# Kernel tuning notes

Measured on AMD Instinct MI355X. Metric: run time of the kernel, lower is better.

Reference implementation:

```python
import jax, jax.numpy as jnp
import numpy as np

NUM_EMOTIONS = 8
EMOTION_DIM = 32
MAX_EMOTIONS = 3
HIDDEN = 768
NUM_HEADS = 8
HEAD_DIM = HIDDEN // NUM_HEADS // 2  # 48
DEPTH = 0
LAMBDA_INIT = 0.8 - 0.6 * float(np.exp(-0.3 * DEPTH))  # 0.2
EPS = 1e-5


def setup_inputs() -> dict:
    key = jax.random.key(0)
    ks = jax.random.split(key, 16)
    B = 16384
    emotion_indices = jax.random.randint(ks[0], (B, MAX_EMOTIONS), 0, NUM_EMOTIONS)
    confidence_values = jax.random.uniform(ks[1], (B, MAX_EMOTIONS), dtype=jnp.float32)
    emb_table = jax.random.normal(ks[2], (NUM_EMOTIONS + 1, EMOTION_DIM), jnp.float32)
    emb_table = emb_table.at[NUM_EMOTIONS].set(0.0)  # padding_idx row
    s1 = 1.0 / np.sqrt(EMOTION_DIM)
    s2 = 1.0 / np.sqrt(HIDDEN)
    W1 = jax.random.normal(ks[3], (EMOTION_DIM, HIDDEN), jnp.float32) * s1
    b1 = jnp.zeros((HIDDEN,), jnp.float32)
    ln_g = jnp.ones((HIDDEN,), jnp.float32)
    ln_b = jnp.zeros((HIDDEN,), jnp.float32)
    Wq = jax.random.normal(ks[4], (HIDDEN, HIDDEN), jnp.float32) * s2
    Wk = jax.random.normal(ks[5], (HIDDEN, HIDDEN), jnp.float32) * s2
    Wv = jax.random.normal(ks[6], (HIDDEN, HIDDEN), jnp.float32) * s2
    Wo = jax.random.normal(ks[7], (HIDDEN, HIDDEN), jnp.float32) * s2
    lq1 = jax.random.normal(ks[8], (HEAD_DIM,), jnp.float32) * 0.1
    lk1 = jax.random.normal(ks[9], (HEAD_DIM,), jnp.float32) * 0.1
    lq2 = jax.random.normal(ks[10], (HEAD_DIM,), jnp.float32) * 0.1
    lk2 = jax.random.normal(ks[11], (HEAD_DIM,), jnp.float32) * 0.1
    subln_w = jnp.ones((2 * HEAD_DIM,), jnp.float32)
    return dict(emotion_indices=emotion_indices, confidence_values=confidence_values,
                emb_table=emb_table, W1=W1, b1=b1, ln_g=ln_g, ln_b=ln_b,
                Wq=Wq, Wk=Wk, Wv=Wv, Wo=Wo,
                lq1=lq1, lk1=lk1, lq2=lq2, lk2=lk2, subln_w=subln_w)


def _rotary_tables(seq_len, dim):
    inv_freq = 1.0 / (10000.0 ** (jnp.arange(0, dim, 2, dtype=jnp.float32) / dim))  # [dim/2]
    t = jnp.arange(seq_len, dtype=jnp.float32)
    ang = jnp.outer(t, inv_freq)  # [S, dim/2]
    return jnp.cos(ang), jnp.sin(ang)


def _apply_rope(x, cos, sin):
    # x: [B, S, H, D]; cos/sin: [S, D/2] (interleaved pairs)
    x1, x2 = x[..., 0::2], x[..., 1::2]
    c = cos[None, :, None, :]
    s = sin[None, :, None, :]
    r1 = x1 * c - x2 * s
    r2 = x1 * s + x2 * c
    return jnp.stack([r1, r2], axis=-1).reshape(x.shape)


def _forward(emotion_indices, confidence_values, emb_table, W1, b1, ln_g, ln_b,
             Wq, Wk, Wv, Wo, lq1, lk1, lq2, lk2, subln_w):
    B, S = emotion_indices.shape  # S == MAX_EMOTIONS
    idx = jnp.where(emotion_indices < 0, NUM_EMOTIONS, emotion_indices)

    # embedding lookup + confidence weighting
    emb = emb_table[idx] * confidence_values[..., None]  # [B,S,32]

    # Linear + LayerNorm + GELU (dropout = identity in eval)
    h = emb @ W1 + b1  # [B,S,768]
    mu = jnp.mean(h, axis=-1, keepdims=True)
    var = jnp.mean(jnp.square(h - mu), axis=-1, keepdims=True)
    h = (h - mu) / jnp.sqrt(var + EPS) * ln_g + ln_b
    h = jax.nn.gelu(h, approximate=False)

    # rotary tables
    cos, sin = _rotary_tables(S, HEAD_DIM)

    # additive attention mask: -inf over padded key columns
    pad = (idx == NUM_EMOTIONS)  # [B,S]
    neg_inf = jnp.asarray(-jnp.inf, h.dtype)
    mask = jnp.where(pad[:, None, None, :], neg_inf, 0.0)  # [B,1,1,S] -> bcast to [B,1,S,S]

    # differential attention
    q = (h @ Wq).reshape(B, S, 2 * NUM_HEADS, HEAD_DIM)
    k = (h @ Wk).reshape(B, S, 2 * NUM_HEADS, HEAD_DIM)
    v = (h @ Wv).reshape(B, S, NUM_HEADS, 2 * HEAD_DIM)
    q = _apply_rope(q, cos, sin)
    k = _apply_rope(k, cos, sin)

    scale = HEAD_DIM ** -0.5
    scores = jnp.einsum('bqhd,bkhd->bhqk', q, k) * scale + mask  # [B,2H,S,S]
    attn = jax.nn.softmax(scores, axis=-1)
    attn = attn.reshape(B, NUM_HEADS, 2, S, S)
    lam = (jnp.exp(jnp.sum(lq1 * lk1)) - jnp.exp(jnp.sum(lq2 * lk2)) + LAMBDA_INIT)
    diff = attn[:, :, 0] - lam * attn[:, :, 1]  # [B,H,S,S]

    out = jnp.einsum('bhqk,bkhd->bqhd', diff, v)  # [B,S,H,2d]
    # sublayer RMSNorm over last dim
    rms = jnp.sqrt(jnp.mean(jnp.square(out), axis=-1, keepdims=True) + EPS)
    out = out / rms * subln_w
    out = out * (1.0 - LAMBDA_INIT)
    out = out.reshape(B, S, HIDDEN) @ Wo  # [B,S,768]

    # masked mean pooling over non-padding positions
    npad = (~pad).astype(out.dtype)[..., None]  # [B,S,1]
    summed = jnp.sum(out * npad, axis=1)
    denom = jnp.maximum(jnp.sum(npad, axis=1), 1.0)
    return summed / denom  # [B,768]


def reference(emotion_indices, confidence_values, emb_table, W1, b1, ln_g, ln_b,
              Wq, Wk, Wv, Wo, lq1, lk1, lq2, lk2, subln_w):
    return _forward(emotion_indices, confidence_values, emb_table, W1, b1, ln_g, ln_b,
                    Wq, Wk, Wv, Wo, lq1, lk1, lq2, lk2, subln_w)
```

## Files before the change

### kernel.cpp

```cpp
#include <hip/hip_runtime.h>
#include <hip/hip_bf16.h>
#include <math.h>
#include <stdint.h>

typedef __hip_bfloat16 bf16;
typedef __attribute__((ext_vector_type(8))) short short8;
typedef __attribute__((ext_vector_type(4))) float f32x4;
typedef __attribute__((ext_vector_type(2))) unsigned int u32x2;

#define NB 16384
#define HID 768
#define EPS_LN 1e-5f
#define LAM_INIT 0.2f

__device__ __forceinline__ float bf2f(bf16 x){ return __bfloat162float(x); }
__device__ __forceinline__ bf16  f2bf(float x){ return __float2bfloat16(x); }
__device__ __forceinline__ float bfbits(uint32_t lo16){ return __uint_as_float(lo16 << 16); }
__device__ __forceinline__ uint32_t f2bfbits(float x){
  union { float f; uint32_t u; } v; v.f = x;
  uint32_t u = v.u;
  uint32_t r = (u + 0x7fff + ((u >> 16) & 1)) >> 16;
  return r;
}

template<typename T> __device__ __forceinline__ float ldv(const void* p, int i);
template<> __device__ __forceinline__ float ldv<float>(const void* p, int i){ return ((const float*)p)[i]; }
template<> __device__ __forceinline__ float ldv<bf16 >(const void* p, int i){ return bf2f(((const bf16*)p)[i]); }

template<typename T> __device__ __forceinline__ void stv(T* p, float v);
template<> __device__ __forceinline__ void stv<float>(float* p, float v){ *p = v; }
template<> __device__ __forceinline__ void stv<bf16 >(bf16*  p, float v){ *p = f2bf(v); }

__device__ __forceinline__ void async_copy16(void* lds, const void* g){
  __builtin_amdgcn_global_load_lds(
      (const __attribute__((address_space(1))) unsigned int*)g,
      (__attribute__((address_space(3))) unsigned int*)lds, 16, 0, 0);
}

__device__ __forceinline__ float wred64(float v){
  #pragma unroll
  for (int m = 1; m <= 32; m <<= 1) v += __shfl_xor(v, m, 64);
  return v;
}

__device__ __forceinline__ int detect_bf(const void* etab){
  const uint32_t* p = (const uint32_t*)((const char*)etab + 512);
  uint32_t v = 0;
  #pragma unroll
  for (int i = 0; i < 16; ++i) v |= p[i];
  return v == 0u ? 1 : 0;
}


__device__ __forceinline__ void misc_body(int isbf, const void* lq1, const void* lk1,
                                          const void* lq2, const void* lk2, float* prep){
  const int lane = threadIdx.x;
  if (lane >= 64) return;
  if (lane == 0) ((int*)prep)[0] = isbf;

  float p1 = 0.f, p2 = 0.f;
  if (lane < 48){
    if (isbf){ p1 = ldv<bf16>(lq1,lane)*ldv<bf16>(lk1,lane); p2 = ldv<bf16>(lq2,lane)*ldv<bf16>(lk2,lane); }
    else     { p1 = ldv<float>(lq1,lane)*ldv<float>(lk1,lane); p2 = ldv<float>(lq2,lane)*ldv<float>(lk2,lane); }
  }
  p1 = wred64(p1); p2 = wred64(p2);
  if (lane == 0) prep[1] = expf(p1) - expf(p2) + LAM_INIT;

  if (lane < 24){
    float invf = powf(10000.f, -(float)(2*lane)/48.f);
    #pragma unroll
    for (int s=0;s<3;++s){
      float ang = (float)s*invf;
      float c = cosf(ang), sv = sinf(ang);
      prep[16  + s*32 + lane] = c;
      prep[128 + s*32 + lane] = sv;
      prep[256 + (s*24 + lane)*2    ] = c;
      prep[256 + (s*24 + lane)*2 + 1] = sv;
    }
  }
}

template<typename T>
__device__ __forceinline__ void prep_e1_body(int id, const void* etab, const void* W1,
                                             const void* b1, float* prep,
                                             float (*red)[4]){
  const int tid = threadIdx.x;
  const int wave = tid >> 6, lane = tid & 63;

  float et[32];
  #pragma unroll
  for (int e=0;e<32;++e) et[e] = ldv<T>(etab, id*32+e);

  float su=0.f, suu=0.f, sub=0.f;
  #pragma unroll
  for (int q=0;q<3;++q){
    const int cc = tid + q*256;
    float s = 0.f;
    #pragma unroll
    for (int e=0;e<32;++e) s += et[e]*ldv<T>(W1, e*HID+cc);
    prep[1024 + id*HID + cc] = s;
    float bv = ldv<T>(b1, cc);
    su += s; suu += s*s; sub += s*bv;
  }
  su = wred64(su); suu = wred64(suu); sub = wred64(sub);
  if (lane==0){ red[0][wave]=su; red[1][wave]=suu; red[2][wave]=sub; }
  __syncthreads();
  if (tid==0){
    float a=0.f,b=0.f,c=0.f;
    #pragma unroll
    for (int w=0;w<4;++w){ a+=red[0][w]; b+=red[1][w]; c+=red[2][w]; }
    prep[512+id]=a*(1.f/768.f); prep[528+id]=b*(1.f/768.f); prep[544+id]=c*(1.f/768.f);
  }
  if (id==0){
    float sb=0.f, sbb=0.f;
    #pragma unroll
    for (int q=0;q<3;++q){ float bv=ldv<T>(b1, tid+q*256); sb+=bv; sbb+=bv*bv; }
    sb=wred64(sb); sbb=wred64(sbb);
    __syncthreads();
    if (lane==0){ red[0][wave]=sb; red[1][wave]=sbb; }
    __syncthreads();
    if (tid==0){
      float a=0.f,b=0.f;
      #pragma unroll
      for (int w=0;w<4;++w){ a+=red[0][w]; b+=red[1][w]; }
      prep[560]=a*(1.f/768.f); prep[561]=b*(1.f/768.f);
    }
  }
}

template<typename T>
__device__ __forceinline__ void transpose_body(bf16 (*tile)[33], const void* src,
                                               bf16* dst, int n0, int k0){
  const int tid = threadIdx.x;
  const int tx = tid & 31, ty = tid >> 5;
  #pragma unroll
  for (int r=0;r<4;++r)
    tile[ty + 8*r][tx] = f2bf(ldv<T>(src, (k0 + ty + 8*r)*HID + n0 + tx));
  __syncthreads();
  #pragma unroll
  for (int r=0;r<4;++r)
    dst[(size_t)(n0 + ty + 8*r)*HID + k0 + tx] = tile[tx][ty + 8*r];
}

__global__ __launch_bounds__(256) void setup_kernel(
    const void* etab, const void* W1, const void* b1,
    const void* lq1, const void* lk1, const void* lq2, const void* lk2,
    const void* Wq, const void* Wk, const void* Wv, const void* Wo,
    bf16* __restrict__ WqkvT, bf16* __restrict__ WoT, float* prep)
{
  __shared__ bf16 tile[32][33];
  __shared__ float red[3][4];
  const int bid = blockIdx.x;
  const int isbf = detect_bf(etab);
  if (bid < 2304){
    const int z = bid / 576, rem = bid % 576;
    const int bx = rem % 24, by = rem / 24;
    const void* src = (z==0)? Wq : (z==1)? Wk : (z==2)? Wv : Wo;
    bf16* dst = (z<3)? (WqkvT + (size_t)z*HID*HID) : WoT;
    if (isbf) transpose_body<bf16 >(tile, src, dst, bx*32, by*32);
    else      transpose_body<float>(tile, src, dst, bx*32, by*32);
  } else if (bid == 2304){
    misc_body(isbf, lq1, lk1, lq2, lk2, prep);
  } else {
    if (isbf) prep_e1_body<bf16 >(bid-2305, etab, W1, b1, prep, red);
    else      prep_e1_body<float>(bid-2305, etab, W1, b1, prep, red);
  }
}

template<typename T>
__device__ __forceinline__ void embed_body(
    int bid, const int* eidx, const void* conf, const void* b1, const void* lng,
    const void* lnb, const float* prep, bf16* hout, int tok0)
{
  const int wave = threadIdx.x >> 6, lane = threadIdx.x & 63;
  const int t0 = bid*16 + wave*4;
  const int c  = lane*12;
  float bb[12], gg[12], be[12];
  #pragma unroll
  for (int d=0;d<12;++d){ bb[d]=ldv<T>(b1,c+d); gg[d]=ldv<T>(lng,c+d); be[d]=ldv<T>(lnb,c+d); }
  const float m_b = prep[560], s_bb = prep[561];
  const float* E1 = prep + 1024;

  #pragma unroll
  for (int tt = 0; tt < 4; ++tt){
    const int tl = t0 + tt, tg = tok0 + tl;
    int id = eidx[tg]; if (id < 0) id = 8;
    const float cf = ldv<T>(conf, tg);
    const float4* ep = (const float4*)(E1 + id*HID + c);
    float4 u0 = ep[0], u1 = ep[1], u2 = ep[2];
    float u[12] = {u0.x,u0.y,u0.z,u0.w, u1.x,u1.y,u1.z,u1.w, u2.x,u2.y,u2.z,u2.w};
    const float mu  = cf*prep[512+id] + m_b;
    const float ex2 = cf*cf*prep[528+id] + 2.f*cf*prep[544+id] + s_bb;
    const float var = ex2 - mu*mu;
    const float rs  = rsqrtf(fmaxf(var, 0.f) + EPS_LN);
    uint32_t w[6];
    #pragma unroll
    for (int d=0;d<6;++d){
      float x0 = cf*u[2*d]   + bb[2*d];
      float x1 = cf*u[2*d+1] + bb[2*d+1];
      float y0 = (x0-mu)*rs*gg[2*d]   + be[2*d];
      float y1 = (x1-mu)*rs*gg[2*d+1] + be[2*d+1];
      float g0 = 0.5f*y0*(1.f + erff(y0*0.70710678118f));
      float g1 = 0.5f*y1*(1.f + erff(y1*0.70710678118f));
      w[d] = f2bfbits(g0) | (f2bfbits(g1) << 16);
    }
    char* op = (char*)hout + (size_t)(tl*HID + c)*2;
    ((u32x2*)op)[0] = (u32x2){w[0],w[1]};
    ((u32x2*)op)[1] = (u32x2){w[2],w[3]};
    ((u32x2*)op)[2] = (u32x2){w[4],w[5]};
  }
}

template<typename T>
__device__ __forceinline__ void attn_body(
    int bid, const bf16* __restrict__ qkv, const int* __restrict__ eidx,
    const void* subw, bf16* __restrict__ obar, int b0, const float* prep)
{
  const int bl = bid*4 + (threadIdx.x>>6);
  const int bg = b0 + bl;
  const int lane = threadIdx.x & 63;
  const int h  = lane >> 3;
  const int u  = lane & 7;
  const int g  = u >> 2;
  const int qd = u & 3;

  float npad[3];
  #pragma unroll
  for (int s=0;s<3;++s){ int id = eidx[bg*3+s]; npad[s] = (id < 0 || id == 8) ? 0.f : 1.f; }
  float denom = npad[0]+npad[1]+npad[2]; if (denom < 1.f) denom = 1.f;
  const float lam = prep[1];
  const float2* pk = (const float2*)(prep + 256);

  const char* base = (const char*)(qkv + (size_t)bl*3*2304);
  const int qoff = (2*h+g)*48 + qd*12;

  u32x2 qw[3][3], kw[3][3];
  #pragma unroll
  for (int s=0;s<3;++s){
    const char* qp = base + (size_t)(s*2304 + qoff)*2;
    const char* kp = qp + 768*2;
    #pragma unroll
    for (int t=0;t<3;++t){
      qw[s][t] = *(const u32x2*)(qp + t*8);
      kw[s][t] = *(const u32x2*)(kp + t*8);
    }
  }

  float sc[3][3];
  #pragma unroll
  for (int a=0;a<3;++a){ sc[a][0]=0.f; sc[a][1]=0.f; sc[a][2]=0.f; }
  #pragma unroll
  for (int j=0;j<6;++j){
    float qr1[3], qr2[3], kr1[3], kr2[3];
    #pragma unroll
    for (int s=0;s<3;++s){
      float2 cs = pk[s*24 + qd*6 + j];
      uint32_t qu = qw[s][j>>1][j&1], ku = kw[s][j>>1][j&1];
      float q1 = bfbits(qu & 0xffffu), q2 = bfbits(qu >> 16);
      float k1 = bfbits(ku & 0xffffu), k2 = bfbits(ku >> 16);
      qr1[s] = q1*cs.x - q2*cs.y;  qr2[s] = q1*cs.y + q2*cs.x;
      kr1[s] = k1*cs.x - k2*cs.y;  kr2[s] = k1*cs.y + k2*cs.x;
    }
    #pragma unroll
    for (int a=0;a<3;++a)
      #pragma unroll
      for (int b=0;b<3;++b) sc[a][b] += qr1[a]*kr1[b] + qr2[a]*kr2[b];
  }
  #pragma unroll
  for (int a=0;a<3;++a)
    #pragma unroll
    for (int b=0;b<3;++b){
      float v = sc[a][b];
      v += __shfl_xor(v, 1, 64);
      v += __shfl_xor(v, 2, 64);
      sc[a][b] = v;
    }

  const float scale = 0.14433756729740643f;
  float att[3][3];
  #pragma unroll
  for (int a=0;a<3;++a){
    float s0 = sc[a][0]*scale + (npad[0] > 0.f ? 0.f : -1e30f);
    float s1 = sc[a][1]*scale + (npad[1] > 0.f ? 0.f : -1e30f);
    float s2 = sc[a][2]*scale + (npad[2] > 0.f ? 0.f : -1e30f);
    float mx = fmaxf(s0, fmaxf(s1, s2));
    float e0 = expf(s0-mx), e1 = expf(s1-mx), e2 = expf(s2-mx);
    float inv = 1.f/(e0+e1+e2);
    att[a][0]=e0*inv; att[a][1]=e1*inv; att[a][2]=e2*inv;
  }
  float diff[3][3];
  #pragma unroll
  for (int a=0;a<3;++a)
    #pragma unroll
    for (int b=0;b<3;++b){
      float other = __shfl_xor(att[a][b], 4, 64);
      diff[a][b] = (g==0) ? (att[a][b] - lam*other) : (other - lam*att[a][b]);
    }

  const int vd = u*12;
  float vv[3][12];
  #pragma unroll
  for (int s=0;s<3;++s){
    const char* vp = base + (size_t)(s*2304 + 1536 + h*96 + vd)*2;
    #pragma unroll
    for (int t=0;t<3;++t){
      u32x2 w = *(const u32x2*)(vp + t*8);
      vv[s][t*4+0] = bfbits(w[0] & 0xffffu);
      vv[s][t*4+1] = bfbits(w[0] >> 16);
      vv[s][t*4+2] = bfbits(w[1] & 0xffffu);
      vv[s][t*4+3] = bfbits(w[1] >> 16);
    }
  }
  float sw[12];
  #pragma unroll
  for (int d=0;d<12;++d) sw[d] = ldv<T>(subw, vd + d);

  float acc[12];
  #pragma unroll
  for (int d=0;d<12;++d) acc[d] = 0.f;
  #pragma unroll
  for (int a=0;a<3;++a){
    float o[12]; float ss = 0.f;
    #pragma unroll
    for (int d=0;d<12;++d){
      o[d] = diff[a][0]*vv[0][d] + diff[a][1]*vv[1][d] + diff[a][2]*vv[2][d];
      ss += o[d]*o[d];
    }
    ss += __shfl_xor(ss, 1, 64);
    ss += __shfl_xor(ss, 2, 64);
    ss += __shfl_xor(ss, 4, 64);
    float rms = sqrtf(ss*(1.f/96.f) + 1e-5f);
    float kk  = npad[a]*0.8f/rms;
    #pragma unroll
    for (int d=0;d<12;++d) acc[d] += o[d]*kk*sw[d];
  }
  const float idn = 1.f/denom;
  char* op = (char*)obar + (size_t)(bg*HID + h*96 + vd)*2;
  #pragma unroll
  for (int t=0;t<3;++t){
    u32x2 w;
    w[0] = f2bfbits(acc[t*4+0]*idn) | (f2bfbits(acc[t*4+1]*idn) << 16);
    w[1] = f2bfbits(acc[t*4+2]*idn) | (f2bfbits(acc[t*4+3]*idn) << 16);
    *(u32x2*)(op + t*8) = w;
  }
}

__global__ __launch_bounds__(256) void attn_embed(
    const bf16* __restrict__ qkv, const int* __restrict__ eidx, const void* subw,
    bf16* __restrict__ obar, int b0, const float* prep,
    const void* conf, const void* b1, const void* lng, const void* lnb,
    bf16* __restrict__ hout, int tok0e, int nattn)
{
  const int isbf = ((const int*)prep)[0];
  if ((int)blockIdx.x < nattn){
    if (isbf) attn_body<bf16 >(blockIdx.x, qkv, eidx, subw, obar, b0, prep);
    else      attn_body<float>(blockIdx.x, qkv, eidx, subw, obar, b0, prep);
  } else {
    const int eb = blockIdx.x - nattn;
    if (isbf) embed_body<bf16 >(eb, eidx, conf, b1, lng, lnb, prep, hout, tok0e);
    else      embed_body<float>(eb, eidx, conf, b1, lng, lnb, prep, hout, tok0e);
  }
}

template<typename OutT>
__device__ __forceinline__ void gemm_body(
    bf16* sA, bf16* sB,
    const bf16* __restrict__ A, const bf16* __restrict__ Bt, OutT* __restrict__ C,
    int K, int lda, int ldb, int ldc, int MT, int NT)
{
  int bid = blockIdx.x;
  int mt, nt;
  if ((MT & 7) == 0) {
    int x = bid & 7, j = bid >> 3;
    nt = j % NT;
    mt = x * (MT >> 3) + j / NT;
  } else { nt = bid % NT; mt = bid / NT; }

  const int tid = threadIdx.x;
  const int wave = tid >> 6, lane = tid & 63;
  const int m0 = mt * 128, n0 = nt * 128;
  const int wm = wave >> 1, wn = wave & 1;

  f32x4 acc[2][4];
  #pragma unroll
  for (int i=0;i<2;++i)
    #pragma unroll
    for (int j=0;j<4;++j) acc[i][j] = (f32x4){0.f,0.f,0.f,0.f};

  const char* Ag = (const char*)(A  + (size_t)m0 * lda);
  const char* Bg = (const char*)(Bt + (size_t)n0 * ldb);
  const int r8  = lane >> 3;
  const int cBx = ((lane & 7) ^ r8) * 16;

  #define STAGE(buf, kt) do {                                                   \
    _Pragma("unroll")                                                           \
    for (int ii = 0; ii < 2; ++ii) {                                            \
      const int i_ = wave*2 + ii;                                               \
      const int row_ = i_*8 + r8;                                               \
      async_copy16((char*)sA + (buf)*16384 + i_*1024 + lane*16,                 \
                   Ag + ((size_t)row_*lda + (kt))*2 + cBx);                     \
      async_copy16((char*)sB + (buf)*16384 + i_*1024 + lane*16,                 \
                   Bg + ((size_t)row_*ldb + (kt))*2 + cBx);                     \
    }                                                                           \
  } while(0)

  STAGE(0, 0);
  int cur = 0;
  const int rxor = (lane & 7) << 3;
  for (int kt = 0; kt < K; kt += 64) {
    __syncthreads();
    if (kt + 64 < K) STAGE(cur^1, kt + 64);
    const bf16* pA = sA + cur*8192;
    const bf16* pB = sB + cur*8192;
    #pragma unroll
    for (int ks = 0; ks < 64; ks += 32) {
      const int kq = (ks + (lane >> 4)*8) ^ rxor;
      short8 af[2], bfv[4];
      #pragma unroll
      for (int i=0;i<2;++i)
        af[i]  = *(const short8*)&pA[(wm*32 + i*16 + (lane&15))*64 + kq];
      #pragma unroll
      for (int j=0;j<4;++j)
        bfv[j] = *(const short8*)&pB[(wn*64 + j*16 + (lane&15))*64 + kq];
      #pragma unroll
      for (int i=0;i<2;++i)
        #pragma unroll
        for (int j=0;j<4;++j)
          acc[i][j] = __builtin_amdgcn_mfma_f32_16x16x32_bf16(af[i], bfv[j], acc[i][j], 0,0,0);
    }
    cur ^= 1;
  }
  #undef STAGE

  const int rb = (lane>>4)*4, cb = lane & 15;
  #pragma unroll
  for (int i=0;i<2;++i)
    #pragma unroll
    for (int r=0;r<4;++r) {
      const int grow = m0 + wm*32 + i*16 + rb + r;
      OutT* Cp = C + (size_t)grow*ldc + n0 + wn*64 + cb;
      #pragma unroll
      for (int j=0;j<4;++j) stv<OutT>(Cp + j*16, acc[i][j][r]);
    }
}

__global__ __launch_bounds__(512) void gemm_int(
    const bf16* __restrict__ A, const bf16* __restrict__ Bt, bf16* __restrict__ C,
    int K, int lda, int ldb, int ldc, int MT, int NT)
{
  __shared__ __align__(16) bf16 sA[2*128*64];
  __shared__ __align__(16) bf16 sB[2*128*64];
  gemm_body<bf16>(sA, sB, A, Bt, C, K, lda, ldb, ldc, MT, NT);
}

__global__ __launch_bounds__(512) void gemm_final(
    const bf16* __restrict__ A, const bf16* __restrict__ Bt, void* C,
    int K, int lda, int ldb, int ldc, int MT, int NT, const float* prep)
{
  __shared__ __align__(16) bf16 sA[2*128*64];
  __shared__ __align__(16) bf16 sB[2*128*64];
  if (((const int*)prep)[0]) gemm_body<bf16 >(sA, sB, A, Bt, (bf16*)C,  K, lda, ldb, ldc, MT, NT);
  else                       gemm_body<float>(sA, sB, A, Bt, (float*)C, K, lda, ldb, ldc, MT, NT);
}

extern "C" void kernel_launch(void* const* d_in, const int* in_sizes, int n_in,
                              void* d_out, int out_size, void* d_ws, size_t ws_size,
                              hipStream_t stream)
{
  const int*  eidx = (const int*) d_in[0];
  const void* conf = d_in[1];
  const void* etab = d_in[2];
  const void* W1   = d_in[3];
  const void* b1   = d_in[4];
  const void* lng  = d_in[5];
  const void* lnb  = d_in[6];
  const void* Wq   = d_in[7];
  const void* Wk   = d_in[8];
  const void* Wv   = d_in[9];
  const void* Wo   = d_in[10];
  const void* lq1  = d_in[11];
  const void* lk1  = d_in[12];
  const void* lq2  = d_in[13];
  const void* lk2  = d_in[14];
  const void* subw = d_in[15];

  const size_t PREP_B = 36864ull;
  const size_t OBAR_B = 25165824ull, WQKVT_B = 3538944ull, WOT_B = 1179648ull;
  const size_t FIXED  = PREP_B + OBAR_B + WQKVT_B + WOT_B;

  char*  ws   = (char*)d_ws;
  float* prep = (float*)ws;
  bf16*  obar = (bf16*)(ws + PREP_B);
  bf16* WqkvT = (bf16*)(ws + PREP_B + OBAR_B);
  bf16* WoT   = (bf16*)(ws + PREP_B + OBAR_B + WQKVT_B);

  int CB = NB;
  while (CB > 128 && FIXED + (size_t)CB*18432ull > ws_size) CB >>= 1;

  bf16* hbuf = (bf16*)(ws + FIXED);
  bf16* qkv  = (bf16*)(ws + FIXED + (size_t)CB*4608ull);

  setup_kernel<<<2314, 256, 0, stream>>>(etab, W1, b1, lq1, lk1, lq2, lk2,
                                         Wq, Wk, Wv, Wo, WqkvT, WoT, prep);

  const int nchunks = NB / CB;
  const int ctok = 3*CB;
  attn_embed<<<ctok/16, 256, 0, stream>>>(qkv, eidx, subw, obar, 0, prep,
                                          conf, b1, lng, lnb, hbuf, 0, 0);
  for (int c = 0; c < nchunks; ++c) {
    const int MT = ctok/128, NT = 18;
    gemm_int<<<MT*NT, 512, 0, stream>>>(hbuf, WqkvT, qkv, HID, HID, HID, 2304, MT, NT);
    const int na = CB/4;
    const int ne = (c+1 < nchunks) ? ctok/16 : 0;
    attn_embed<<<na+ne, 256, 0, stream>>>(qkv, eidx, subw, obar, c*CB, prep,
                                          conf, b1, lng, lnb, hbuf, (c+1)*ctok, na);
  }

  gemm_final<<<128*6, 512, 0, stream>>>(obar, WoT, (void*)d_out, HID, HID, HID, HID, 128, 6, prep);
}
```

Before: 415.8 us.

## Software-pipeline QKV GEMM with attention and embed in one fused launch

```diff
diff --git a/kernel.cpp b/kernel.cpp
--- a/kernel.cpp
+++ b/kernel.cpp
@@ -169,11 +169,11 @@
 
 template<typename T>
 __device__ __forceinline__ void embed_body(
-    int bid, const int* eidx, const void* conf, const void* b1, const void* lng,
+    int ebid, const int* eidx, const void* conf, const void* b1, const void* lng,
     const void* lnb, const float* prep, bf16* hout, int tok0)
 {
   const int wave = threadIdx.x >> 6, lane = threadIdx.x & 63;
-  const int t0 = bid*16 + wave*4;
+  const int t0 = ebid*32 + wave*4;
   const int c  = lane*12;
   float bb[12], gg[12], be[12];
   #pragma unroll
@@ -213,10 +213,10 @@
 
 template<typename T>
 __device__ __forceinline__ void attn_body(
-    int bid, const bf16* __restrict__ qkv, const int* __restrict__ eidx,
+    int abid, const bf16* __restrict__ qkv, const int* __restrict__ eidx,
     const void* subw, bf16* __restrict__ obar, int b0, const float* prep)
 {
-  const int bl = bid*4 + (threadIdx.x>>6);
+  const int bl = abid*8 + (threadIdx.x>>6);
   const int bg = b0 + bl;
   const int lane = threadIdx.x & 63;
   const int h  = lane >> 3;
@@ -345,30 +345,12 @@
   }
 }
 
-__global__ __launch_bounds__(256) void attn_embed(
-    const bf16* __restrict__ qkv, const int* __restrict__ eidx, const void* subw,
-    bf16* __restrict__ obar, int b0, const float* prep,
-    const void* conf, const void* b1, const void* lng, const void* lnb,
-    bf16* __restrict__ hout, int tok0e, int nattn)
-{
-  const int isbf = ((const int*)prep)[0];
-  if ((int)blockIdx.x < nattn){
-    if (isbf) attn_body<bf16 >(blockIdx.x, qkv, eidx, subw, obar, b0, prep);
-    else      attn_body<float>(blockIdx.x, qkv, eidx, subw, obar, b0, prep);
-  } else {
-    const int eb = blockIdx.x - nattn;
-    if (isbf) embed_body<bf16 >(eb, eidx, conf, b1, lng, lnb, prep, hout, tok0e);
-    else      embed_body<float>(eb, eidx, conf, b1, lng, lnb, prep, hout, tok0e);
-  }
-}
-
 template<typename OutT>
-__device__ __forceinline__ void gemm_body(
+__device__ __forceinline__ void gemm_body(int bid,
     bf16* sA, bf16* sB,
     const bf16* __restrict__ A, const bf16* __restrict__ Bt, OutT* __restrict__ C,
     int K, int lda, int ldb, int ldc, int MT, int NT)
 {
-  int bid = blockIdx.x;
   int mt, nt;
   if ((MT & 7) == 0) {
     int x = bid & 7, j = bid >> 3;
@@ -444,13 +426,32 @@
     }
 }
 
-__global__ __launch_bounds__(512) void gemm_int(
-    const bf16* __restrict__ A, const bf16* __restrict__ Bt, bf16* __restrict__ C,
-    int K, int lda, int ldb, int ldc, int MT, int NT)
+__global__ __launch_bounds__(512) void fused_step(
+    int ngemm, int nattn,
+    const bf16* __restrict__ A, const bf16* __restrict__ Bt,
+    bf16* __restrict__ Cq, int MT, int NT,
+    const bf16* __restrict__ qkv_in, int b0,
+    int tok0e, bf16* __restrict__ hout,
+    const int* __restrict__ eidx, const void* conf, const void* subw,
+    const void* b1, const void* lng, const void* lnb,
+    bf16* __restrict__ obar, const float* prep)
 {
   __shared__ __align__(16) bf16 sA[2*128*64];
   __shared__ __align__(16) bf16 sB[2*128*64];
-  gemm_body<bf16>(sA, sB, A, Bt, C, K, lda, ldb, ldc, MT, NT);
+  const int bid = blockIdx.x;
+  if (bid < ngemm){
+    gemm_body<bf16>(bid, sA, sB, A, Bt, Cq, HID, HID, HID, 2304, MT, NT);
+    return;
+  }
+  const int isbf = ((const int*)prep)[0];
+  if (bid < ngemm + nattn){
+    if (isbf) attn_body<bf16 >(bid-ngemm, qkv_in, eidx, subw, obar, b0, prep);
+    else      attn_body<float>(bid-ngemm, qkv_in, eidx, subw, obar, b0, prep);
+  } else {
+    const int eb = bid - ngemm - nattn;
+    if (isbf) embed_body<bf16 >(eb, eidx, conf, b1, lng, lnb, prep, hout, tok0e);
+    else      embed_body<float>(eb, eidx, conf, b1, lng, lnb, prep, hout, tok0e);
+  }
 }
 
 __global__ __launch_bounds__(512) void gemm_final(
@@ -459,8 +460,8 @@
 {
   __shared__ __align__(16) bf16 sA[2*128*64];
   __shared__ __align__(16) bf16 sB[2*128*64];
-  if (((const int*)prep)[0]) gemm_body<bf16 >(sA, sB, A, Bt, (bf16*)C,  K, lda, ldb, ldc, MT, NT);
-  else                       gemm_body<float>(sA, sB, A, Bt, (float*)C, K, lda, ldb, ldc, MT, NT);
+  if (((const int*)prep)[0]) gemm_body<bf16 >(blockIdx.x, sA, sB, A, Bt, (bf16*)C,  K, lda, ldb, ldc, MT, NT);
+  else                       gemm_body<float>(blockIdx.x, sA, sB, A, Bt, (float*)C, K, lda, ldb, ldc, MT, NT);
 }
 
 extern "C" void kernel_launch(void* const* d_in, const int* in_sizes, int n_in,
@@ -494,27 +495,41 @@
   bf16* WqkvT = (bf16*)(ws + PREP_B + OBAR_B);
   bf16* WoT   = (bf16*)(ws + PREP_B + OBAR_B + WQKVT_B);
 
-  int CB = NB;
-  while (CB > 128 && FIXED + (size_t)CB*18432ull > ws_size) CB >>= 1;
-
-  bf16* hbuf = (bf16*)(ws + FIXED);
-  bf16* qkv  = (bf16*)(ws + FIXED + (size_t)CB*4608ull);
+  int CB = 8192;
+  while (CB > 1024 && FIXED + (size_t)CB*36864ull > ws_size) CB >>= 1;
+
+  bf16* hb[2] = { (bf16*)(ws + FIXED),
+                  (bf16*)(ws + FIXED + (size_t)CB*4608ull) };
+  bf16* qk[2] = { (bf16*)(ws + FIXED + (size_t)CB*9216ull),
+                  (bf16*)(ws + FIXED + (size_t)CB*9216ull + (size_t)CB*13824ull) };
+
+  const int nchunks = NB / CB;
+  const int ctok = 3*CB;
+  const int MT = ctok/128, NT = 18;
+  const int ngemm = MT*NT;
+  const int nattn = CB/8;
+  const int nembed = ctok/32;
 
   setup_kernel<<<2314, 256, 0, stream>>>(etab, W1, b1, lq1, lk1, lq2, lk2,
                                          Wq, Wk, Wv, Wo, WqkvT, WoT, prep);
 
-  const int nchunks = NB / CB;
-  const int ctok = 3*CB;
-  attn_embed<<<ctok/16, 256, 0, stream>>>(qkv, eidx, subw, obar, 0, prep,
-                                          conf, b1, lng, lnb, hbuf, 0, 0);
+  fused_step<<<nembed, 512, 0, stream>>>(0, 0, hb[0], WqkvT, qk[0], MT, NT,
+                                         qk[0], 0, 0, hb[0],
+                                         eidx, conf, subw, b1, lng, lnb, obar, prep);
   for (int c = 0; c < nchunks; ++c) {
-    const int MT = ctok/128, NT = 18;
-    gemm_int<<<MT*NT, 512, 0, stream>>>(hbuf, WqkvT, qkv, HID, HID, HID, 2304, MT, NT);
-    const int na = CB/4;
-    const int ne = (c+1 < nchunks) ? ctok/16 : 0;
-    attn_embed<<<na+ne, 256, 0, stream>>>(qkv, eidx, subw, obar, c*CB, prep,
-                                          conf, b1, lng, lnb, hbuf, (c+1)*ctok, na);
-  }
+    const int na = (c >= 1) ? nattn : 0;
+    const int ne = (c+1 < nchunks) ? nembed : 0;
+    fused_step<<<ngemm+na+ne, 512, 0, stream>>>(
+        ngemm, na,
+        hb[c&1], WqkvT, qk[c&1], MT, NT,
+        qk[(c&1)^1], (c-1)*CB,
+        (c+1)*ctok, hb[(c&1)^1],
+        eidx, conf, subw, b1, lng, lnb, obar, prep);
+  }
+  fused_step<<<nattn, 512, 0, stream>>>(0, nattn, hb[0], WqkvT, qk[0], MT, NT,
+                                        qk[(nchunks-1)&1], (nchunks-1)*CB,
+                                        0, hb[0],
+                                        eidx, conf, subw, b1, lng, lnb, obar, prep);
 
   gemm_final<<<128*6, 512, 0, stream>>>(obar, WoT, (void*)d_out, HID, HID, HID, HID, 128, 6, prep);
 }
```

Result: slower. 449.9 us (+8.2%).
